# Kernel optimization log

Hardware: AMD Instinct MI355X
Metric: run time of the kernel (lower is better)

## Reference

```python
import jax, jax.numpy as jnp
import numpy as np

N = 100_000          # nodes
E = 3_200_000        # edges (avg degree 32)
IN = 128             # input feature dim
H = 4                # heads
D = 16               # out feats per head
NEG_SLOPE = 0.2


def setup_inputs() -> dict:
    key = jax.random.key(0)
    ks = jax.random.split(key, 7)
    h = jax.random.normal(ks[0], (N, IN), dtype=jnp.float32)
    W = jax.random.normal(ks[1], (H * D, IN), dtype=jnp.float32) * (1.0 / np.sqrt(IN))
    attn_l = jax.random.normal(ks[2], (H, D), dtype=jnp.float32) * 0.1
    attn_r = jax.random.normal(ks[3], (H, D), dtype=jnp.float32) * 0.1
    bias = jax.random.normal(ks[4], (H * D,), dtype=jnp.float32) * 0.01
    src = jax.random.randint(ks[5], (E,), 0, N, dtype=jnp.int32)
    dst = jax.random.randint(ks[6], (E,), 0, N, dtype=jnp.int32)
    return {"h": h, "W": W, "attn_l": attn_l, "attn_r": attn_r,
            "bias": bias, "src": src, "dst": dst}


def reference(h, W, attn_l, attn_r, bias, src, dst):
    # Linear projection: [N, IN] @ [IN, H*D] -> [N, H, D]
    feat = (h @ W.T).reshape(N, H, D)
    # Per-node attention logits (a_l^T Wh_src, a_r^T Wh_dst): [N, H]
    el = jnp.einsum('nhd,hd->nh', feat, attn_l)
    er = jnp.einsum('nhd,hd->nh', feat, attn_r)
    # Edge scores with LeakyReLU: [E, H]
    e = el[src] + er[dst]
    e = jnp.where(e > 0, e, NEG_SLOPE * e)
    # Segment softmax over incoming edges of each destination node
    m = jax.ops.segment_max(e, dst, num_segments=N)          # [N, H]
    m = jnp.where(jnp.isfinite(m), m, 0.0)                   # empty segments
    ex = jnp.exp(e - m[dst])                                 # [E, H]
    s = jax.ops.segment_sum(ex, dst, num_segments=N)         # [N, H]
    alpha = ex / jnp.where(s[dst] > 0, s[dst], 1.0)          # [E, H]
    # Weighted scatter-sum aggregation: [E, H, D] messages -> [N, H, D]
    msg = feat[src] * alpha[:, :, None]
    out = jax.ops.segment_sum(msg, dst, num_segments=N)
    out = out + bias.reshape(1, H, D)
    return out
```

## Files before the change

kernel.cpp:

```cpp
#include <hip/hip_runtime.h>

#define N_NODES 100000
#define N_EDGES 3200000
#define IN_DIM  128
#define HEADS   4
#define OUT_DIM 64
#define NEG_SLOPE 0.2f

#define BSH   9
#define BNOD  (1 << BSH)
#define BMSK  (BNOD - 1)
#define NBUCK 196
#define MAXB  19456
#define CHUNK 8192
#define NCHUNK 391
#define BPAD  16
#define NGEMMB 1563

typedef __attribute__((ext_vector_type(8))) short bf16x8;
typedef __attribute__((ext_vector_type(4))) float f32x4;

__device__ inline unsigned short f2bf_rne(float x) {
    unsigned u = __float_as_uint(x);
    u += 0x7FFFu + ((u >> 16) & 1u);
    return (unsigned short)(u >> 16);
}
__device__ inline float wsum64(float v) {
    #pragma unroll
    for (int o = 32; o; o >>= 1) v += __shfl_xor(v, o);
    return v;
}

__global__ __launch_bounds__(256) void gat_prep(
    const float* __restrict__ W, unsigned short* __restrict__ Whi,
    unsigned short* __restrict__ Wlo, int* __restrict__ bcur)
{
    const int i = blockIdx.x * 256 + threadIdx.x;
    if (i < NBUCK) bcur[i * BPAD] = i * MAXB;
    if (i < OUT_DIM * IN_DIM) {
        const float w = W[i];
        const unsigned short hi = f2bf_rne(w);
        const float whif = __uint_as_float((unsigned)hi << 16);
        Whi[i] = hi;
        Wlo[i] = f2bf_rne(w - whif);
    }
}

__global__ __launch_bounds__(256) void gat_gb(
    const float* __restrict__ h,
    const unsigned short* __restrict__ Whi, const unsigned short* __restrict__ Wlo,
    const float* __restrict__ attn_l, const float* __restrict__ attn_r,
    unsigned short* __restrict__ featbf, float* __restrict__ el, float* __restrict__ er,
    const int* __restrict__ src, const int* __restrict__ dst,
    int* __restrict__ bcur, unsigned int* __restrict__ binned)
{
    __shared__ int cnt[NBUCK];
    __shared__ int boff[NBUCK];
    const int tid = threadIdx.x;

    if (blockIdx.x < NGEMMB) {
        const int w    = tid >> 6;
        const int lane = tid & 63;
        const int row  = lane & 15;
        const int kg   = lane >> 4;
        const int n0   = blockIdx.x * 64 + w * 16;

        int gn = n0 + row; if (gn >= N_NODES) gn = N_NODES - 1;
        const float* hrow = h + (size_t)gn * IN_DIM;

        bf16x8 ahi[4], alo[4];
        #pragma unroll
        for (int kc = 0; kc < 4; ++kc) {
            const float4 f0 = *reinterpret_cast<const float4*>(hrow + kc * 32 + kg * 8);
            const float4 f1 = *reinterpret_cast<const float4*>(hrow + kc * 32 + kg * 8 + 4);
            const float f[8] = {f0.x, f0.y, f0.z, f0.w, f1.x, f1.y, f1.z, f1.w};
            #pragma unroll
            for (int j = 0; j < 8; ++j) {
                const unsigned short hi = f2bf_rne(f[j]);
                const float hif = __uint_as_float((unsigned)hi << 16);
                ahi[kc][j] = (short)hi;
                alo[kc][j] = (short)f2bf_rne(f[j] - hif);
            }
        }

        f32x4 acc[4];
        #pragma unroll
        for (int ob = 0; ob < 4; ++ob) acc[ob] = (f32x4){0.f, 0.f, 0.f, 0.f};

        #pragma unroll
        for (int kc = 0; kc < 4; ++kc) {
            #pragma unroll
            for (int ob = 0; ob < 4; ++ob) {
                const size_t woff = (size_t)(ob * 16 + row) * IN_DIM + kc * 32 + kg * 8;
                const bf16x8 bhi = *reinterpret_cast<const bf16x8*>(Whi + woff);
                const bf16x8 blo = *reinterpret_cast<const bf16x8*>(Wlo + woff);
                acc[ob] = __builtin_amdgcn_mfma_f32_16x16x32_bf16(ahi[kc], bhi, acc[ob], 0, 0, 0);
                acc[ob] = __builtin_amdgcn_mfma_f32_16x16x32_bf16(ahi[kc], blo, acc[ob], 0, 0, 0);
                acc[ob] = __builtin_amdgcn_mfma_f32_16x16x32_bf16(alo[kc], bhi, acc[ob], 0, 0, 0);
            }
        }

        float alv[4], arv[4];
        #pragma unroll
        for (int ob = 0; ob < 4; ++ob) {
            alv[ob] = attn_l[ob * 16 + row];
            arv[ob] = attn_r[ob * 16 + row];
        }
        #pragma unroll
        for (int ob = 0; ob < 4; ++ob) {
            #pragma unroll
            for (int reg = 0; reg < 4; ++reg) {
                const int node = n0 + kg * 4 + reg;
                float vl = acc[ob][reg] * alv[ob];
                float vr = acc[ob][reg] * arv[ob];
                #pragma unroll
                for (int off = 1; off < 16; off <<= 1) {
                    vl += __shfl_xor(vl, off);
                    vr += __shfl_xor(vr, off);
                }
                if (row == 0 && node < N_NODES) {
                    el[node * 4 + ob] = vl;
                    er[node * 4 + ob] = vr;
                }
                const unsigned bfv = (unsigned)f2bf_rne(acc[ob][reg]);
                const unsigned pw = (unsigned)__shfl_xor((int)bfv, 1);
                if (!(lane & 1) && node < N_NODES) {
                    *reinterpret_cast<unsigned*>(featbf + (size_t)node * OUT_DIM + ob * 16 + row) =
                        (bfv & 0xFFFFu) | (pw << 16);
                }
            }
        }
    } else {
        const int base = (blockIdx.x - NGEMMB) * CHUNK;
        const int nval = min(CHUNK, N_EDGES - base);

        if (tid < NBUCK) cnt[tid] = 0;
        __syncthreads();
        for (int i = tid; i < nval; i += 256)
            atomicAdd(&cnt[dst[base + i] >> BSH], 1);
        __syncthreads();
        if (tid < NBUCK) {
            int c2 = cnt[tid];
            boff[tid] = c2 ? atomicAdd(&bcur[tid * BPAD], c2) : 0;
        }
        __syncthreads();
        for (int i = tid; i < nval; i += 256) {
            int d = dst[base + i], s = src[base + i];
            int k = d >> BSH;
            int slot = atomicAdd(&boff[k], 1);
            int lim = (k + 1) * MAXB - 1;
            if (slot > lim) slot = lim;
            binned[slot] = ((unsigned)s << BSH) | (unsigned)(d & BMSK);
        }
    }
}

__global__ __launch_bounds__(1024) void gat_sortb(
    const unsigned int* __restrict__ binned, const int* __restrict__ bcur,
    int* __restrict__ csr, int* __restrict__ nbeg, int* __restrict__ nend)
{
    __shared__ int lhist[BNOD];
    __shared__ int lcur[BNOD];
    __shared__ int wtot[8];
    const int b = blockIdx.x;
    const int tid = threadIdx.x;
    const int nodebase = b << BSH;
    const int beg = b * MAXB;
    const int end = min(bcur[b * BPAD], beg + MAXB);

    if (tid < BNOD) lhist[tid] = 0;
    __syncthreads();
    for (int i = beg + tid; i < end; i += 1024)
        atomicAdd(&lhist[binned[i] & BMSK], 1);
    __syncthreads();

    int v = 0, inc = 0;
    if (tid < BNOD) {
        v = lhist[tid];
        inc = v;
        #pragma unroll
        for (int off = 1; off < 64; off <<= 1) {
            int t = __shfl_up(inc, off, 64);
            if ((tid & 63) >= off) inc += t;
        }
        if ((tid & 63) == 63) wtot[tid >> 6] = inc;
    }
    __syncthreads();
    if (tid < 8) {
        int t = wtot[tid];
        int inc2 = t;
        #pragma unroll
        for (int off = 1; off < 8; off <<= 1) {
            int u = __shfl_up(inc2, off, 64);
            if (tid >= off) inc2 += u;
        }
        wtot[tid] = inc2 - t;
    }
    __syncthreads();
    if (tid < BNOD) {
        const int incl = inc + wtot[tid >> 6];
        const int e0 = incl - v;
        lcur[tid] = e0;
        const int n = nodebase + tid;
        if (n < N_NODES) { nbeg[n] = beg + e0; nend[n] = beg + incl; }
    }
    __syncthreads();
    for (int i = beg + tid; i < end; i += 1024) {
        const unsigned u = binned[i];
        const int pos = atomicAdd(&lcur[u & BMSK], 1);
        csr[beg + pos] = (int)(u >> BSH);
    }
}

__global__ __launch_bounds__(256) void gat_agg(
    const int* __restrict__ nbeg, const int* __restrict__ nend,
    const int* __restrict__ csr,
    const float* __restrict__ el, const float* __restrict__ er,
    const unsigned short* __restrict__ featbf, const float* __restrict__ bias,
    float* __restrict__ out)
{
    __shared__ float pb[4][4 * 68];
    __shared__ int   sb[4][64];
    const int w = threadIdx.x >> 6;
    const int n = blockIdx.x * 4 + w;
    if (n >= N_NODES) return;
    const int lane = threadIdx.x & 63;
    const int eo = lane >> 4;
    const int cs = lane & 15;
    const int hh = cs >> 2;

    const float4 er4 = *reinterpret_cast<const float4*>(er + n * 4);
    const float4 b4  = *reinterpret_cast<const float4*>(bias + 4 * cs);
    const int beg = nbeg[n], end = nend[n];

    float ss0 = 0.f, ss1 = 0.f, ss2 = 0.f, ss3 = 0.f;
    float a0 = 0.f, a1 = 0.f, a2 = 0.f, a3 = 0.f;

    int mysrc = (beg + lane < end) ? csr[beg + lane] : 0;

    for (int c = beg; c < end; c += 64) {
        const int nv = min(64, end - c);
        const bool act = lane < nv;
        const int nidx = c + 64 + lane;
        const int nxt = (nidx < end) ? csr[nidx] : 0;

        const float4 el4 = *reinterpret_cast<const float4*>(el + mysrc * 4);
        float sc0 = el4.x + er4.x, sc1 = el4.y + er4.y;
        float sc2 = el4.z + er4.z, sc3 = el4.w + er4.w;
        sc0 = sc0 > 0.f ? sc0 : NEG_SLOPE * sc0;
        sc1 = sc1 > 0.f ? sc1 : NEG_SLOPE * sc1;
        sc2 = sc2 > 0.f ? sc2 : NEG_SLOPE * sc2;
        sc3 = sc3 > 0.f ? sc3 : NEG_SLOPE * sc3;
        if (!act) { sc0 = sc1 = sc2 = sc3 = -1e30f; }

        const float p0 = __expf(sc0), p1 = __expf(sc1);
        const float p2 = __expf(sc2), p3 = __expf(sc3);
        ss0 += p0; ss1 += p1; ss2 += p2; ss3 += p3;

        pb[w][0 * 68 + lane] = p0;
        pb[w][1 * 68 + lane] = p1;
        pb[w][2 * 68 + lane] = p2;
        pb[w][3 * 68 + lane] = p3;
        sb[w][lane] = mysrc;

        const int steps = (nv + 3) >> 2;
        #pragma unroll 4
        for (int j = 0; j < steps; ++j) {
            const int e4 = 4 * j + eo;
            const int s  = sb[w][e4];
            const float p = pb[w][hh * 68 + e4];
            const uint2 q = *reinterpret_cast<const uint2*>(
                featbf + (size_t)s * OUT_DIM + 4 * cs);
            a0 = fmaf(p, __uint_as_float(q.x << 16),          a0);
            a1 = fmaf(p, __uint_as_float(q.x & 0xFFFF0000u),  a1);
            a2 = fmaf(p, __uint_as_float(q.y << 16),          a2);
            a3 = fmaf(p, __uint_as_float(q.y & 0xFFFF0000u),  a3);
        }
        mysrc = nxt;
    }

    a0 += __shfl_xor(a0, 16); a0 += __shfl_xor(a0, 32);
    a1 += __shfl_xor(a1, 16); a1 += __shfl_xor(a1, 32);
    a2 += __shfl_xor(a2, 16); a2 += __shfl_xor(a2, 32);
    a3 += __shfl_xor(a3, 16); a3 += __shfl_xor(a3, 32);

    const float t0 = wsum64(ss0), t1 = wsum64(ss1);
    const float t2 = wsum64(ss2), t3 = wsum64(ss3);
    const float sv = hh == 0 ? t0 : hh == 1 ? t1 : hh == 2 ? t2 : t3;
    const float inv = 1.f / (sv > 0.f ? sv : 1.f);

    if (eo == 0) {
        float4 o4;
        o4.x = a0 * inv + b4.x; o4.y = a1 * inv + b4.y;
        o4.z = a2 * inv + b4.z; o4.w = a3 * inv + b4.w;
        *reinterpret_cast<float4*>(out + (size_t)n * OUT_DIM + 4 * cs) = o4;
    }
}

extern "C" void kernel_launch(void* const* d_in, const int* in_sizes, int n_in,
                              void* d_out, int out_size, void* d_ws, size_t ws_size,
                              hipStream_t stream) {
    const float* h      = (const float*)d_in[0];
    const float* W      = (const float*)d_in[1];
    const float* attn_l = (const float*)d_in[2];
    const float* attn_r = (const float*)d_in[3];
    const float* bias   = (const float*)d_in[4];
    const int*   src    = (const int*)d_in[5];
    const int*   dst    = (const int*)d_in[6];
    float* out = (float*)d_out;

    unsigned short* featbf = (unsigned short*)d_ws;
    float* el   = (float*)(featbf + (size_t)N_NODES * OUT_DIM);
    float* er   = el + (size_t)N_NODES * HEADS;
    unsigned short* Whi = (unsigned short*)(er + (size_t)N_NODES * HEADS);
    unsigned short* Wlo = Whi + OUT_DIM * IN_DIM;
    int*   bcur = (int*)(Wlo + OUT_DIM * IN_DIM);
    unsigned int* binned = (unsigned int*)(bcur + NBUCK * BPAD + 16);
    int*   csr  = (int*)(binned + (size_t)NBUCK * MAXB);
    int*   nbeg = csr + (size_t)NBUCK * MAXB;
    int*   nend = nbeg + N_NODES;

    gat_prep<<<32, 256, 0, stream>>>(W, Whi, Wlo, bcur);
    gat_gb<<<NGEMMB + NCHUNK, 256, 0, stream>>>(h, Whi, Wlo, attn_l, attn_r,
                                                featbf, el, er, src, dst, bcur, binned);
    gat_sortb<<<NBUCK, 1024, 0, stream>>>(binned, bcur, csr, nbeg, nend);
    gat_agg<<<(N_NODES + 3) / 4, 256, 0, stream>>>(nbeg, nend, csr, el, er, featbf, bias, out);
}
```

Baseline: 165.3 us.

## Split GEMM from edge binning and stage binned edges in LDS for coalesced writes

Splits the fused GEMM and edge-binning kernel into two separate launches. The binning kernel now computes a block-local prefix scan of bucket counts, scatters edges into shared memory grouped by bucket, and then copies each bucket's run contiguously to global memory with wave-wide writes. Previously each edge was scattered straight to global memory. The aim is to replace random global stores with coalesced ones. In exchange it adds an extra kernel launch, gives up overlap between GEMM and binning blocks, and uses 32KB of LDS per binning block, which lowers occupancy.

```diff
diff --git a/kernel.cpp b/kernel.cpp
--- a/kernel.cpp
+++ b/kernel.cpp
@@ -15,7 +15,6 @@
 #define CHUNK 8192
 #define NCHUNK 391
 #define BPAD  16
-#define NGEMMB 1563
 
 typedef __attribute__((ext_vector_type(8))) short bf16x8;
 typedef __attribute__((ext_vector_type(4))) float f32x4;
@@ -46,111 +45,150 @@
     }
 }
 
-__global__ __launch_bounds__(256) void gat_gb(
+__global__ __launch_bounds__(256) void gat_gemm(
     const float* __restrict__ h,
     const unsigned short* __restrict__ Whi, const unsigned short* __restrict__ Wlo,
     const float* __restrict__ attn_l, const float* __restrict__ attn_r,
-    unsigned short* __restrict__ featbf, float* __restrict__ el, float* __restrict__ er,
+    unsigned short* __restrict__ featbf, float* __restrict__ el, float* __restrict__ er)
+{
+    const int tid  = threadIdx.x;
+    const int w    = tid >> 6;
+    const int lane = tid & 63;
+    const int row  = lane & 15;
+    const int kg   = lane >> 4;
+    const int n0   = blockIdx.x * 64 + w * 16;
+
+    int gn = n0 + row; if (gn >= N_NODES) gn = N_NODES - 1;
+    const float* hrow = h + (size_t)gn * IN_DIM;
+
+    bf16x8 ahi[4], alo[4];
+    #pragma unroll
+    for (int kc = 0; kc < 4; ++kc) {
+        const float4 f0 = *reinterpret_cast<const float4*>(hrow + kc * 32 + kg * 8);
+        const float4 f1 = *reinterpret_cast<const float4*>(hrow + kc * 32 + kg * 8 + 4);
+        const float f[8] = {f0.x, f0.y, f0.z, f0.w, f1.x, f1.y, f1.z, f1.w};
+        #pragma unroll
+        for (int j = 0; j < 8; ++j) {
+            const unsigned short hi = f2bf_rne(f[j]);
+            const float hif = __uint_as_float((unsigned)hi << 16);
+            ahi[kc][j] = (short)hi;
+            alo[kc][j] = (short)f2bf_rne(f[j] - hif);
+        }
+    }
+
+    f32x4 acc[4];
+    #pragma unroll
+    for (int ob = 0; ob < 4; ++ob) acc[ob] = (f32x4){0.f, 0.f, 0.f, 0.f};
+
+    #pragma unroll
+    for (int kc = 0; kc < 4; ++kc) {
+        #pragma unroll
+        for (int ob = 0; ob < 4; ++ob) {
+            const size_t woff = (size_t)(ob * 16 + row) * IN_DIM + kc * 32 + kg * 8;
+            const bf16x8 bhi = *reinterpret_cast<const bf16x8*>(Whi + woff);
+            const bf16x8 blo = *reinterpret_cast<const bf16x8*>(Wlo + woff);
+            acc[ob] = __builtin_amdgcn_mfma_f32_16x16x32_bf16(ahi[kc], bhi, acc[ob], 0, 0, 0);
+            acc[ob] = __builtin_amdgcn_mfma_f32_16x16x32_bf16(ahi[kc], blo, acc[ob], 0, 0, 0);
+            acc[ob] = __builtin_amdgcn_mfma_f32_16x16x32_bf16(alo[kc], bhi, acc[ob], 0, 0, 0);
+        }
+    }
+
+    float alv[4], arv[4];
+    #pragma unroll
+    for (int ob = 0; ob < 4; ++ob) {
+        alv[ob] = attn_l[ob * 16 + row];
+        arv[ob] = attn_r[ob * 16 + row];
+    }
+    #pragma unroll
+    for (int ob = 0; ob < 4; ++ob) {
+        #pragma unroll
+        for (int reg = 0; reg < 4; ++reg) {
+            const int node = n0 + kg * 4 + reg;
+            float vl = acc[ob][reg] * alv[ob];
+            float vr = acc[ob][reg] * arv[ob];
+            #pragma unroll
+            for (int off = 1; off < 16; off <<= 1) {
+                vl += __shfl_xor(vl, off);
+                vr += __shfl_xor(vr, off);
+            }
+            if (row == 0 && node < N_NODES) {
+                el[node * 4 + ob] = vl;
+                er[node * 4 + ob] = vr;
+            }
+            const unsigned bfv = (unsigned)f2bf_rne(acc[ob][reg]);
+            const unsigned pw = (unsigned)__shfl_xor((int)bfv, 1);
+            if (!(lane & 1) && node < N_NODES) {
+                *reinterpret_cast<unsigned*>(featbf + (size_t)node * OUT_DIM + ob * 16 + row) =
+                    (bfv & 0xFFFFu) | (pw << 16);
+            }
+        }
+    }
+}
+
+__global__ __launch_bounds__(256) void gat_bin(
     const int* __restrict__ src, const int* __restrict__ dst,
     int* __restrict__ bcur, unsigned int* __restrict__ binned)
 {
     __shared__ int cnt[NBUCK];
     __shared__ int boff[NBUCK];
-    const int tid = threadIdx.x;
-
-    if (blockIdx.x < NGEMMB) {
-        const int w    = tid >> 6;
-        const int lane = tid & 63;
-        const int row  = lane & 15;
-        const int kg   = lane >> 4;
-        const int n0   = blockIdx.x * 64 + w * 16;
-
-        int gn = n0 + row; if (gn >= N_NODES) gn = N_NODES - 1;
-        const float* hrow = h + (size_t)gn * IN_DIM;
-
-        bf16x8 ahi[4], alo[4];
-        #pragma unroll
-        for (int kc = 0; kc < 4; ++kc) {
-            const float4 f0 = *reinterpret_cast<const float4*>(hrow + kc * 32 + kg * 8);
-            const float4 f1 = *reinterpret_cast<const float4*>(hrow + kc * 32 + kg * 8 + 4);
-            const float f[8] = {f0.x, f0.y, f0.z, f0.w, f1.x, f1.y, f1.z, f1.w};
-            #pragma unroll
-            for (int j = 0; j < 8; ++j) {
-                const unsigned short hi = f2bf_rne(f[j]);
-                const float hif = __uint_as_float((unsigned)hi << 16);
-                ahi[kc][j] = (short)hi;
-                alo[kc][j] = (short)f2bf_rne(f[j] - hif);
-            }
-        }
-
-        f32x4 acc[4];
-        #pragma unroll
-        for (int ob = 0; ob < 4; ++ob) acc[ob] = (f32x4){0.f, 0.f, 0.f, 0.f};
-
-        #pragma unroll
-        for (int kc = 0; kc < 4; ++kc) {
-            #pragma unroll
-            for (int ob = 0; ob < 4; ++ob) {
-                const size_t woff = (size_t)(ob * 16 + row) * IN_DIM + kc * 32 + kg * 8;
-                const bf16x8 bhi = *reinterpret_cast<const bf16x8*>(Whi + woff);
-                const bf16x8 blo = *reinterpret_cast<const bf16x8*>(Wlo + woff);
-                acc[ob] = __builtin_amdgcn_mfma_f32_16x16x32_bf16(ahi[kc], bhi, acc[ob], 0, 0, 0);
-                acc[ob] = __builtin_amdgcn_mfma_f32_16x16x32_bf16(ahi[kc], blo, acc[ob], 0, 0, 0);
-                acc[ob] = __builtin_amdgcn_mfma_f32_16x16x32_bf16(alo[kc], bhi, acc[ob], 0, 0, 0);
-            }
-        }
-
-        float alv[4], arv[4];
-        #pragma unroll
-        for (int ob = 0; ob < 4; ++ob) {
-            alv[ob] = attn_l[ob * 16 + row];
-            arv[ob] = attn_r[ob * 16 + row];
-        }
-        #pragma unroll
-        for (int ob = 0; ob < 4; ++ob) {
-            #pragma unroll
-            for (int reg = 0; reg < 4; ++reg) {
-                const int node = n0 + kg * 4 + reg;
-                float vl = acc[ob][reg] * alv[ob];
-                float vr = acc[ob][reg] * arv[ob];
-                #pragma unroll
-                for (int off = 1; off < 16; off <<= 1) {
-                    vl += __shfl_xor(vl, off);
-                    vr += __shfl_xor(vr, off);
-                }
-                if (row == 0 && node < N_NODES) {
-                    el[node * 4 + ob] = vl;
-                    er[node * 4 + ob] = vr;
-                }
-                const unsigned bfv = (unsigned)f2bf_rne(acc[ob][reg]);
-                const unsigned pw = (unsigned)__shfl_xor((int)bfv, 1);
-                if (!(lane & 1) && node < N_NODES) {
-                    *reinterpret_cast<unsigned*>(featbf + (size_t)node * OUT_DIM + ob * 16 + row) =
-                        (bfv & 0xFFFFu) | (pw << 16);
-                }
-            }
-        }
-    } else {
-        const int base = (blockIdx.x - NGEMMB) * CHUNK;
-        const int nval = min(CHUNK, N_EDGES - base);
-
-        if (tid < NBUCK) cnt[tid] = 0;
-        __syncthreads();
-        for (int i = tid; i < nval; i += 256)
-            atomicAdd(&cnt[dst[base + i] >> BSH], 1);
-        __syncthreads();
-        if (tid < NBUCK) {
-            int c2 = cnt[tid];
-            boff[tid] = c2 ? atomicAdd(&bcur[tid * BPAD], c2) : 0;
-        }
-        __syncthreads();
-        for (int i = tid; i < nval; i += 256) {
-            int d = dst[base + i], s = src[base + i];
-            int k = d >> BSH;
-            int slot = atomicAdd(&boff[k], 1);
-            int lim = (k + 1) * MAXB - 1;
-            if (slot > lim) slot = lim;
-            binned[slot] = ((unsigned)s << BSH) | (unsigned)(d & BMSK);
+    __shared__ int lofs[NBUCK];
+    __shared__ int lcur[NBUCK];
+    __shared__ int wt[4];
+    __shared__ unsigned es[CHUNK];
+    const int tid  = threadIdx.x;
+    const int base = blockIdx.x * CHUNK;
+    const int nval = min(CHUNK, N_EDGES - base);
+
+    if (tid < NBUCK) cnt[tid] = 0;
+    __syncthreads();
+    for (int i = tid; i < nval; i += 256)
+        atomicAdd(&cnt[dst[base + i] >> BSH], 1);
+    __syncthreads();
+
+    const int v = (tid < NBUCK) ? cnt[tid] : 0;
+    int inc = v;
+    #pragma unroll
+    for (int off = 1; off < 64; off <<= 1) {
+        int t = __shfl_up(inc, off, 64);
+        if ((tid & 63) >= off) inc += t;
+    }
+    if ((tid & 63) == 63) wt[tid >> 6] = inc;
+    __syncthreads();
+    if (tid < 4) {
+        int t = wt[tid], i2 = t;
+        #pragma unroll
+        for (int off = 1; off < 4; off <<= 1) {
+            int u = __shfl_up(i2, off, 64);
+            if (tid >= off) i2 += u;
+        }
+        wt[tid] = i2 - t;
+    }
+    __syncthreads();
+    if (tid < NBUCK) {
+        const int e0 = inc - v + wt[tid >> 6];
+        lofs[tid] = e0;
+        lcur[tid] = e0;
+        boff[tid] = v ? atomicAdd(&bcur[tid * BPAD], v) : 0;
+    }
+    __syncthreads();
+
+    for (int i = tid; i < nval; i += 256) {
+        const int d = dst[base + i], s = src[base + i];
+        const int k = d >> BSH;
+        const int pos = atomicAdd(&lcur[k], 1);
+        es[pos] = ((unsigned)s << BSH) | (unsigned)(d & BMSK);
+    }
+    __syncthreads();
+
+    const int wv = tid >> 6, ln = tid & 63;
+    for (int k = wv; k < NBUCK; k += 4) {
+        const int lo = lofs[k], len = cnt[k], gb = boff[k];
+        const int lim = (k + 1) * MAXB - (k * MAXB);
+        for (int j = ln; j < len; j += 64) {
+            int gj = gb + j;
+            int gmax = (k + 1) * MAXB - 1;
+            if (gj > gmax) gj = gmax;
+            binned[gj] = es[lo + j];
         }
     }
 }
@@ -321,8 +359,8 @@
     int*   nend = nbeg + N_NODES;
 
     gat_prep<<<32, 256, 0, stream>>>(W, Whi, Wlo, bcur);
-    gat_gb<<<NGEMMB + NCHUNK, 256, 0, stream>>>(h, Whi, Wlo, attn_l, attn_r,
-                                                featbf, el, er, src, dst, bcur, binned);
+    gat_gemm<<<(N_NODES + 63) / 64, 256, 0, stream>>>(h, Whi, Wlo, attn_l, attn_r, featbf, el, er);
+    gat_bin<<<NCHUNK, 256, 0, stream>>>(src, dst, bcur, binned);
     gat_sortb<<<NBUCK, 1024, 0, stream>>>(binned, bcur, csr, nbeg, nend);
     gat_agg<<<(N_NODES + 3) / 4, 256, 0, stream>>>(nbeg, nend, csr, el, er, featbf, bias, out);
 }
```

Measured after the change: 179.9 us. 1.09x slower.
